# Kernel tuning notes

Measured on AMD Instinct MI355X. Metric: run time of the kernel, lower is better.

Reference implementation:

```python
import jax, jax.numpy as jnp
import numpy as np

N, E, F_DIM, H = 50000, 800000, 128, 4


def setup_inputs() -> dict:
    key = jax.random.key(0)
    ks = jax.random.split(key, 12)
    x = jax.random.normal(ks[0], (N, F_DIM), dtype=jnp.float32)
    edge_index = jax.random.randint(ks[1], (2, E), 0, N, dtype=jnp.int64)
    s = 1.0 / np.sqrt(F_DIM)
    return {
        "x": x,
        "edge_index": edge_index,
        "W_gat": jax.random.normal(ks[2], (F_DIM, H * F_DIM), dtype=jnp.float32) * s,
        "att_src": jax.random.normal(ks[3], (H, F_DIM), dtype=jnp.float32) * s,
        "att_dst": jax.random.normal(ks[4], (H, F_DIM), dtype=jnp.float32) * s,
        "bias_gat": jnp.zeros((H * F_DIM,), dtype=jnp.float32),
        "W_mha": jax.random.normal(ks[5], (H * F_DIM, F_DIM), dtype=jnp.float32) * s,
        "b_mha": jnp.zeros((F_DIM,), dtype=jnp.float32),
        "W1": jax.random.normal(ks[6], (F_DIM, F_DIM), dtype=jnp.float32) * s,
        "b1": jnp.zeros((F_DIM,), dtype=jnp.float32),
        "W2": jax.random.normal(ks[7], (F_DIM, F_DIM), dtype=jnp.float32) * s,
        "b2": jnp.zeros((F_DIM,), dtype=jnp.float32),
    }


def gat_conv(x, src, dst, W_gat, att_src, att_dst, bias_gat):
    n = x.shape[0]
    xp = (x @ W_gat).reshape(n, H, F_DIM)            # [N,H,F]
    a_src = jnp.einsum('nhf,hf->nh', xp, att_src)    # [N,H]
    a_dst = jnp.einsum('nhf,hf->nh', xp, att_dst)
    alpha = jax.nn.leaky_relu(a_src[src] + a_dst[dst], 0.2)  # [E,H]
    m = jax.ops.segment_max(alpha, dst, num_segments=n)      # segment softmax over dst
    e = jnp.exp(alpha - m[dst])
    denom = jax.ops.segment_sum(e, dst, num_segments=n)
    att = e / denom[dst]                              # [E,H]
    msg = xp[src] * att[:, :, None]                   # [E,H,F] gather-weight
    out = jax.ops.segment_sum(msg, dst, num_segments=n)  # [N,H,F]
    return out.reshape(n, H * F_DIM) + bias_gat


def reference(x, edge_index, W_gat, att_src, att_dst, bias_gat, W_mha, b_mha, W1, b1, W2, b2):
    n = x.shape[0]
    # PyG GATConv default add_self_loops=True
    ar = jnp.arange(n, dtype=edge_index.dtype)
    src = jnp.concatenate([edge_index[0], ar])
    dst = jnp.concatenate([edge_index[1], ar])
    residual = x
    h = jax.nn.leaky_relu(gat_conv(x, src, dst, W_gat, att_src, att_dst, bias_gat), 0.01)
    h = h @ W_mha + b_mha + residual
    # Ffn
    res2 = h
    h = jax.nn.leaky_relu(h @ W1 + b1, 0.01)
    h = h @ W2 + b2 + res2
    return h
```

## Files before the change

### kernel.cpp

```cpp
#include <hip/hip_runtime.h>

#define FD 128
#define NH 4
#define HF 512
#define CAP 64

typedef __attribute__((ext_vector_type(8))) short short8;
typedef __attribute__((ext_vector_type(4))) float v4f;

__device__ __forceinline__ float lrelu(float x, float s) { return x > 0.f ? x : s * x; }

__device__ __forceinline__ unsigned short f2bf(float f) {
    unsigned int u = __float_as_uint(f);
    u += 0x7FFFu + ((u >> 16) & 1u);
    return (unsigned short)(u >> 16);
}
__device__ __forceinline__ unsigned int pack2(float a, float b) {
    return (unsigned)f2bf(a) | ((unsigned)f2bf(b) << 16);
}

__global__ __launch_bounds__(256) void k_prep(const float* __restrict__ x,
                                              unsigned short* __restrict__ xb,
                                              const float* __restrict__ Wg, unsigned short* __restrict__ WgT,
                                              const float* __restrict__ Wm, unsigned short* __restrict__ WmT,
                                              const float* __restrict__ W1, unsigned short* __restrict__ W1T,
                                              const float* __restrict__ W2, unsigned short* __restrict__ W2T,
                                              const float* __restrict__ att_s,
                                              const float* __restrict__ att_d,
                                              float* __restrict__ U, int n) {
    const int t = threadIdx.x;
    int b = blockIdx.x;
    const int nCast = (n * FD / 8 + 255) / 256;
    const int nT1 = (FD * HF / 4 + 255) / 256;
    const int nT3 = (FD * FD / 4 + 255) / 256;
    if (b < nCast) {
        int i = b * 256 + t;
        if (i < n * FD / 8) {
            const float4* x4 = reinterpret_cast<const float4*>(x);
            float4 v0 = x4[i * 2], v1 = x4[i * 2 + 1];
            uint4 o;
            o.x = pack2(v0.x, v0.y); o.y = pack2(v0.z, v0.w);
            o.z = pack2(v1.x, v1.y); o.w = pack2(v1.z, v1.w);
            reinterpret_cast<uint4*>(xb)[i] = o;
        }
        return;
    }
    b -= nCast;
    if (b < nT1) {
        int i4 = (b * 256 + t) * 4;
        if (i4 < FD * HF) {
            int nn = i4 >> 7, k = i4 & 127;
            uint2 o;
            o.x = pack2(Wg[(size_t)k * HF + nn], Wg[(size_t)(k + 1) * HF + nn]);
            o.y = pack2(Wg[(size_t)(k + 2) * HF + nn], Wg[(size_t)(k + 3) * HF + nn]);
            *reinterpret_cast<uint2*>(&WgT[i4]) = o;
        }
        return;
    }
    b -= nT1;
    if (b < nT1) {
        int i4 = (b * 256 + t) * 4;
        if (i4 < HF * FD) {
            int nn = i4 >> 9, k = i4 & 511;
            uint2 o;
            o.x = pack2(Wm[(size_t)k * FD + nn], Wm[(size_t)(k + 1) * FD + nn]);
            o.y = pack2(Wm[(size_t)(k + 2) * FD + nn], Wm[(size_t)(k + 3) * FD + nn]);
            *reinterpret_cast<uint2*>(&WmT[i4]) = o;
        }
        return;
    }
    b -= nT1;
    if (b < nT3) {
        int i4 = (b * 256 + t) * 4;
        if (i4 < FD * FD) {
            int nn = i4 >> 7, k = i4 & 127;
            uint2 o;
            o.x = pack2(W1[(size_t)k * FD + nn], W1[(size_t)(k + 1) * FD + nn]);
            o.y = pack2(W1[(size_t)(k + 2) * FD + nn], W1[(size_t)(k + 3) * FD + nn]);
            *reinterpret_cast<uint2*>(&W1T[i4]) = o;
        }
        return;
    }
    b -= nT3;
    if (b < nT3) {
        int i4 = (b * 256 + t) * 4;
        if (i4 < FD * FD) {
            int nn = i4 >> 7, k = i4 & 127;
            uint2 o;
            o.x = pack2(W2[(size_t)k * FD + nn], W2[(size_t)(k + 1) * FD + nn]);
            o.y = pack2(W2[(size_t)(k + 2) * FD + nn], W2[(size_t)(k + 3) * FD + nn]);
            *reinterpret_cast<uint2*>(&W2T[i4]) = o;
        }
        return;
    }
    b -= nT3;
    {
        int idx = b * 256 + t;
        if (idx < 1024) {
            int type = idx >> 9, h = (idx >> 7) & 3, k = idx & 127;
            const float* att = type ? att_d : att_s;
            const float* wrow = &Wg[(size_t)k * HF + h * FD];
            const float* arow = &att[h * FD];
            float s = 0.f;
#pragma unroll 4
            for (int j = 0; j < FD; ++j) s += wrow[j] * arow[j];
            U[idx] = s;
        }
    }
}

__global__ __launch_bounds__(256) void k_alog(const unsigned short* __restrict__ xb,
                                              const float* __restrict__ U,
                                              float* __restrict__ a_s,
                                              float* __restrict__ a_d, int n) {
    int idx = blockIdx.x * 256 + threadIdx.x;
    int node = idx >> 2, h = idx & 3;
    if (node >= n) return;
    const uint4* xr = reinterpret_cast<const uint4*>(&xb[(size_t)node * FD]);
    const float* us = &U[h * FD];
    const float* ud = &U[512 + h * FD];
    float ps = 0.f, pd = 0.f;
#pragma unroll 4
    for (int j = 0; j < 16; ++j) {
        uint4 u = xr[j];
        const unsigned w[4] = {u.x, u.y, u.z, u.w};
#pragma unroll
        for (int q = 0; q < 4; ++q) {
            float f0 = __uint_as_float(w[q] << 16);
            float f1 = __uint_as_float(w[q] & 0xffff0000u);
            int c = j * 8 + q * 2;
            ps += f0 * us[c] + f1 * us[c + 1];
            pd += f0 * ud[c] + f1 * ud[c + 1];
        }
    }
    a_s[node * NH + h] = ps;
    a_d[node * NH + h] = pd;
}

__global__ __launch_bounds__(256) void k_scatter(const int* __restrict__ es,
                                                 const int* __restrict__ ed,
                                                 const float* __restrict__ a_s,
                                                 const float* __restrict__ a_d,
                                                 int* __restrict__ cur,
                                                 uint4* __restrict__ edata, int E, int n) {
    int i = blockIdx.x * 256 + threadIdx.x;
    if (i >= E) return;
    int s = es[i], d = ed[i];
    const float4 as = *reinterpret_cast<const float4*>(&a_s[(size_t)s * NH]);
    const float4 ad = *reinterpret_cast<const float4*>(&a_d[(size_t)d * NH]);
    float w0 = __expf(lrelu(as.x + ad.x, 0.2f));
    float w1 = __expf(lrelu(as.y + ad.y, 0.2f));
    float w2 = __expf(lrelu(as.z + ad.z, 0.2f));
    float w3 = __expf(lrelu(as.w + ad.w, 0.2f));
    int pos = atomicAdd(&cur[d], 1);
    if (pos < CAP) {
        uint4 r;
        r.x = (unsigned)s;
        r.y = pack2(w0, w1);
        r.z = pack2(w2, w3);
        r.w = 0u;
        edata[(size_t)d * CAP + pos] = r;
    }
}

#define GATH(REC) (*reinterpret_cast<const unsigned*>(&xb[(size_t)(int)(REC).x * FD + 2 * l]))
#define ACCUM(REC, U) do {                                                     \
    float w0_ = __uint_as_float((REC).y << 16);                                \
    float w1_ = __uint_as_float((REC).y & 0xffff0000u);                        \
    float w2_ = __uint_as_float((REC).z << 16);                                \
    float w3_ = __uint_as_float((REC).z & 0xffff0000u);                        \
    float g0_ = __uint_as_float((U) << 16);                                    \
    float g1_ = __uint_as_float((U) & 0xffff0000u);                            \
    ax0 += g0_ * w0_; ay0 += g1_ * w0_; den0 += w0_;                           \
    ax1 += g0_ * w1_; ay1 += g1_ * w1_; den1 += w1_;                           \
    ax2 += g0_ * w2_; ay2 += g1_ * w2_; den2 += w2_;                           \
    ax3 += g0_ * w3_; ay3 += g1_ * w3_; den3 += w3_;                           \
} while (0)

__global__ __launch_bounds__(256, 8) void k_aggr2(const unsigned short* __restrict__ xb,
                                                  const float* __restrict__ a_s,
                                                  const float* __restrict__ a_d,
                                                  const int* __restrict__ cur,
                                                  const uint4* __restrict__ edata,
                                                  unsigned short* __restrict__ agg, int n) {
    const int wv = threadIdx.x >> 6, l = threadIdx.x & 63;
    const int node = blockIdx.x * 4 + wv;
    if (node >= n) return;
    const int un = __builtin_amdgcn_readfirstlane(node);

    const float4 as4 = *reinterpret_cast<const float4*>(&a_s[(size_t)node * NH]);
    const float4 ad4 = *reinterpret_cast<const float4*>(&a_d[(size_t)node * NH]);
    const float wS0 = __expf(lrelu(as4.x + ad4.x, 0.2f));
    const float wS1 = __expf(lrelu(as4.y + ad4.y, 0.2f));
    const float wS2 = __expf(lrelu(as4.z + ad4.z, 0.2f));
    const float wS3 = __expf(lrelu(as4.w + ad4.w, 0.2f));

    float ax0, ay0, ax1, ay1, ax2, ay2, ax3, ay3;
    float den0 = wS0, den1 = wS1, den2 = wS2, den3 = wS3;
    {
        unsigned ux = *reinterpret_cast<const unsigned*>(&xb[(size_t)node * FD + 2 * l]);
        float f0 = __uint_as_float(ux << 16);
        float f1 = __uint_as_float(ux & 0xffff0000u);
        ax0 = f0 * wS0; ay0 = f1 * wS0;
        ax1 = f0 * wS1; ay1 = f1 * wS1;
        ax2 = f0 * wS2; ay2 = f1 * wS2;
        ax3 = f0 * wS3; ay3 = f1 * wS3;
    }

    const uint4* p = edata + (size_t)un * CAP;
    int dg = __builtin_amdgcn_readfirstlane(cur[un]);
    dg = min(dg, CAP);
    int e = 0;
    for (; e + 8 <= dg; e += 8) {
        uint4 r0 = p[e], r1 = p[e + 1], r2 = p[e + 2], r3 = p[e + 3];
        uint4 r4 = p[e + 4], r5 = p[e + 5], r6 = p[e + 6], r7 = p[e + 7];
        unsigned u0 = GATH(r0), u1 = GATH(r1), u2 = GATH(r2), u3 = GATH(r3);
        unsigned u4 = GATH(r4), u5 = GATH(r5), u6 = GATH(r6), u7 = GATH(r7);
        ACCUM(r0, u0); ACCUM(r1, u1); ACCUM(r2, u2); ACCUM(r3, u3);
        ACCUM(r4, u4); ACCUM(r5, u5); ACCUM(r6, u6); ACCUM(r7, u7);
    }
    if (e + 4 <= dg) {
        uint4 r0 = p[e], r1 = p[e + 1], r2 = p[e + 2], r3 = p[e + 3];
        unsigned u0 = GATH(r0), u1 = GATH(r1), u2 = GATH(r2), u3 = GATH(r3);
        ACCUM(r0, u0); ACCUM(r1, u1); ACCUM(r2, u2); ACCUM(r3, u3);
        e += 4;
    }
    if (e + 2 <= dg) {
        uint4 r0 = p[e], r1 = p[e + 1];
        unsigned u0 = GATH(r0), u1 = GATH(r1);
        ACCUM(r0, u0); ACCUM(r1, u1);
        e += 2;
    }
    if (e < dg) {
        uint4 r0 = p[e];
        unsigned u0 = GATH(r0);
        ACCUM(r0, u0);
    }

    const float i0 = 1.f / den0, i1 = 1.f / den1, i2 = 1.f / den2, i3 = 1.f / den3;
    unsigned* ag = reinterpret_cast<unsigned*>(&agg[(size_t)node * HF + 2 * l]);
    ag[0]   = pack2(ax0 * i0, ay0 * i0);
    ag[64]  = pack2(ax1 * i1, ay1 * i1);
    ag[128] = pack2(ax2 * i2, ay2 * i2);
    ag[192] = pack2(ax3 * i3, ay3 * i3);
}

#define PREFETCH8(BP, STRIDE) do {                                             \
    _Pragma("unroll")                                                          \
    for (int rnd = 0; rnd < 8; ++rnd) {                                        \
        int r_ = rnd * 16 + sr;                                                \
        R[rnd] = *reinterpret_cast<const short8*>(&(BP)[(size_t)r_ * (STRIDE) + sc]); \
    } } while (0)

#define COMMIT8() do {                                                         \
    __syncthreads();                                                           \
    _Pragma("unroll")                                                          \
    for (int rnd = 0; rnd < 8; ++rnd) {                                        \
        int r_ = rnd * 16 + sr;                                                \
        *reinterpret_cast<short8*>(&WL[r_][sc]) = R[rnd];                      \
    }                                                                          \
    __syncthreads(); } while (0)

#define LOAD_A(HH) do {                                                        \
    _Pragma("unroll")                                                          \
    for (int kk = 0; kk < 4; ++kk) {                                           \
        RA0[kk] = *reinterpret_cast<const short8*>(                            \
            &agg[(size_t)amr0 * HF + (HH) * FD + kk * 32 + kg]);               \
        RA1[kk] = *reinterpret_cast<const short8*>(                            \
            &agg[(size_t)amr1 * HF + (HH) * FD + kk * 32 + kg]);               \
    } } while (0)

__global__ __launch_bounds__(256, 2) void k_tail(const unsigned short* __restrict__ agg,
                                                 const unsigned short* __restrict__ WgT,
                                                 const float* __restrict__ biasg,
                                                 const unsigned short* __restrict__ WmT,
                                                 const float* __restrict__ bm,
                                                 const float* __restrict__ x,
                                                 const unsigned short* __restrict__ W1T,
                                                 const float* __restrict__ b1,
                                                 const unsigned short* __restrict__ W2T,
                                                 const float* __restrict__ b2,
                                                 float* __restrict__ out, int n) {
    __shared__ unsigned short WL[128][132];
    __shared__ unsigned short tS[128][132];
    const int tid = threadIdx.x;
    const int m0 = blockIdx.x * 128;
    const int wv = tid >> 6, l = tid & 63;
    const int rA = l & 15;
    const int kg = (l >> 4) * 8;
    const int mw = m0 + wv * 32;
    const int amr0 = min(mw + rA, n - 1);
    const int amr1 = min(mw + 16 + rA, n - 1);
    const int sr = tid >> 4, sc = (tid & 15) * 8;

    short8 R[8];
    short8 RA0[4], RA1[4];
    v4f hma[2][8];
#pragma unroll
    for (int g = 0; g < 2; ++g)
#pragma unroll
        for (int t = 0; t < 8; ++t) hma[g][t] = (v4f){0.f, 0.f, 0.f, 0.f};

    LOAD_A(0);
    PREFETCH8(WgT, FD);

#pragma unroll
    for (int h = 0; h < 4; ++h) {
        COMMIT8();
        PREFETCH8(WmT + h * FD, HF);
        v4f acc[2][8];
#pragma unroll
        for (int g = 0; g < 2; ++g)
#pragma unroll
            for (int t = 0; t < 8; ++t) acc[g][t] = (v4f){0.f, 0.f, 0.f, 0.f};
        __builtin_amdgcn_s_setprio(1);
#pragma unroll
        for (int kk = 0; kk < 4; ++kk) {
#pragma unroll
            for (int nt = 0; nt < 8; ++nt) {
                short8 b = *reinterpret_cast<const short8*>(&WL[nt * 16 + rA][kk * 32 + kg]);
                acc[0][nt] = __builtin_amdgcn_mfma_f32_16x16x32_bf16(RA0[kk], b, acc[0][nt], 0, 0, 0);
                acc[1][nt] = __builtin_amdgcn_mfma_f32_16x16x32_bf16(RA1[kk], b, acc[1][nt], 0, 0, 0);
            }
        }
        __builtin_amdgcn_s_setprio(0);
#pragma unroll
        for (int g = 0; g < 2; ++g)
#pragma unroll
            for (int nt = 0; nt < 8; ++nt) {
                const int col = nt * 16 + rA;
                const float bv = biasg[h * FD + col];
#pragma unroll
                for (int i = 0; i < 4; ++i)
                    tS[wv * 32 + g * 16 + (l >> 4) * 4 + i][col] =
                        f2bf(lrelu(acc[g][nt][i] + bv, 0.01f));
            }
        COMMIT8();
        PREFETCH8((h < 3 ? WgT + (h + 1) * FD * FD : W1T), FD);
        if (h < 3) LOAD_A(h + 1);
        __builtin_amdgcn_s_setprio(1);
#pragma unroll
        for (int kk = 0; kk < 4; ++kk) {
            short8 a0 = *reinterpret_cast<const short8*>(&tS[wv * 32 + rA][kk * 32 + kg]);
            short8 a1 = *reinterpret_cast<const short8*>(&tS[wv * 32 + 16 + rA][kk * 32 + kg]);
#pragma unroll
            for (int nt = 0; nt < 8; ++nt) {
                short8 b = *reinterpret_cast<const short8*>(&WL[nt * 16 + rA][kk * 32 + kg]);
                hma[0][nt] = __builtin_amdgcn_mfma_f32_16x16x32_bf16(a0, b, hma[0][nt], 0, 0, 0);
                hma[1][nt] = __builtin_amdgcn_mfma_f32_16x16x32_bf16(a1, b, hma[1][nt], 0, 0, 0);
            }
        }
        __builtin_amdgcn_s_setprio(0);
    }

#pragma unroll
    for (int g = 0; g < 2; ++g)
#pragma unroll
        for (int nt = 0; nt < 8; ++nt) {
            const int col = nt * 16 + rA;
            const float bv = bm[col];
#pragma unroll
            for (int i = 0; i < 4; ++i) {
                const int r = min(mw + g * 16 + (l >> 4) * 4 + i, n - 1);
                float v = hma[g][nt][i] + bv + x[(size_t)r * FD + col];
                hma[g][nt][i] = v;
                tS[wv * 32 + g * 16 + (l >> 4) * 4 + i][col] = f2bf(v);
            }
        }
    COMMIT8();
    PREFETCH8(W2T, FD);
    v4f acc[2][8];
#pragma unroll
    for (int g = 0; g < 2; ++g)
#pragma unroll
        for (int t = 0; t < 8; ++t) acc[g][t] = (v4f){0.f, 0.f, 0.f, 0.f};
    __builtin_amdgcn_s_setprio(1);
#pragma unroll
    for (int kk = 0; kk < 4; ++kk) {
        short8 a0 = *reinterpret_cast<const short8*>(&tS[wv * 32 + rA][kk * 32 + kg]);
        short8 a1 = *reinterpret_cast<const short8*>(&tS[wv * 32 + 16 + rA][kk * 32 + kg]);
#pragma unroll
        for (int nt = 0; nt < 8; ++nt) {
            short8 b = *reinterpret_cast<const short8*>(&WL[nt * 16 + rA][kk * 32 + kg]);
            acc[0][nt] = __builtin_amdgcn_mfma_f32_16x16x32_bf16(a0, b, acc[0][nt], 0, 0, 0);
            acc[1][nt] = __builtin_amdgcn_mfma_f32_16x16x32_bf16(a1, b, acc[1][nt], 0, 0, 0);
        }
    }
    __builtin_amdgcn_s_setprio(0);
#pragma unroll
    for (int g = 0; g < 2; ++g)
#pragma unroll
        for (int nt = 0; nt < 8; ++nt) {
            const int col = nt * 16 + rA;
            const float bv = b1[col];
#pragma unroll
            for (int i = 0; i < 4; ++i)
                tS[wv * 32 + g * 16 + (l >> 4) * 4 + i][col] =
                    f2bf(lrelu(acc[g][nt][i] + bv, 0.01f));
        }
    COMMIT8();
#pragma unroll
    for (int g = 0; g < 2; ++g)
#pragma unroll
        for (int t = 0; t < 8; ++t) acc[g][t] = (v4f){0.f, 0.f, 0.f, 0.f};
    __builtin_amdgcn_s_setprio(1);
#pragma unroll
    for (int kk = 0; kk < 4; ++kk) {
        short8 a0 = *reinterpret_cast<const short8*>(&tS[wv * 32 + rA][kk * 32 + kg]);
        short8 a1 = *reinterpret_cast<const short8*>(&tS[wv * 32 + 16 + rA][kk * 32 + kg]);
#pragma unroll
        for (int nt = 0; nt < 8; ++nt) {
            short8 b = *reinterpret_cast<const short8*>(&WL[nt * 16 + rA][kk * 32 + kg]);
            acc[0][nt] = __builtin_amdgcn_mfma_f32_16x16x32_bf16(a0, b, acc[0][nt], 0, 0, 0);
            acc[1][nt] = __builtin_amdgcn_mfma_f32_16x16x32_bf16(a1, b, acc[1][nt], 0, 0, 0);
        }
    }
    __builtin_amdgcn_s_setprio(0);
#pragma unroll
    for (int g = 0; g < 2; ++g)
#pragma unroll
        for (int nt = 0; nt < 8; ++nt) {
            const int col = nt * 16 + rA;
            const float bv = b2[col];
#pragma unroll
            for (int i = 0; i < 4; ++i) {
                const int r = mw + g * 16 + (l >> 4) * 4 + i;
                if (r < n)
                    out[(size_t)r * FD + col] = acc[g][nt][i] + bv + hma[g][nt][i];
            }
        }
}

extern "C" void kernel_launch(void* const* d_in, const int* in_sizes, int n_in,
                              void* d_out, int out_size, void* d_ws, size_t ws_size,
                              hipStream_t stream) {
    const float* x     = (const float*)d_in[0];
    const int*   ei    = (const int*)d_in[1];
    const float* Wg    = (const float*)d_in[2];
    const float* att_s = (const float*)d_in[3];
    const float* att_d = (const float*)d_in[4];
    const float* biasg = (const float*)d_in[5];
    const float* Wm    = (const float*)d_in[6];
    const float* bm    = (const float*)d_in[7];
    const float* W1    = (const float*)d_in[8];
    const float* b1    = (const float*)d_in[9];
    const float* W2    = (const float*)d_in[10];
    const float* b2    = (const float*)d_in[11];
    float* out = (float*)d_out;

    const int n = in_sizes[0] / FD;
    const int E = in_sizes[1] / 2;
    const int* esrc = ei;
    const int* edst = ei + E;

    char* w = (char*)d_ws;
    size_t o = 0;
    auto alloc = [&](size_t b) { void* p = w + o; o = (o + b + 255) & ~(size_t)255; return p; };
    unsigned short* x_b  = (unsigned short*)alloc((size_t)n * FD * 2);
    unsigned short* WgT  = (unsigned short*)alloc((size_t)FD * HF * 2);
    unsigned short* WmT  = (unsigned short*)alloc((size_t)HF * FD * 2);
    unsigned short* W1T  = (unsigned short*)alloc((size_t)FD * FD * 2);
    unsigned short* W2T  = (unsigned short*)alloc((size_t)FD * FD * 2);
    float*          U    = (float*)alloc(1024 * 4);
    unsigned short* aggb = (unsigned short*)alloc((size_t)n * HF * 2);
    float* a_s   = (float*)alloc((size_t)n * NH * 4);
    float* a_d   = (float*)alloc((size_t)n * NH * 4);
    int*   cur   = (int*)alloc((size_t)n * 4);
    uint4* edata = (uint4*)alloc((size_t)n * CAP * 16);

    hipMemsetAsync(cur, 0, (size_t)n * 4, stream);

    const int nCast = (n * FD / 8 + 255) / 256;
    const int nT1 = (FD * HF / 4 + 255) / 256;
    const int nT3 = (FD * FD / 4 + 255) / 256;
    k_prep<<<nCast + 2 * nT1 + 2 * nT3 + 4, 256, 0, stream>>>(
        x, x_b, Wg, WgT, Wm, WmT, W1, W1T, W2, W2T, att_s, att_d, U, n);

    k_alog<<<(n * 4 + 255) / 256, 256, 0, stream>>>(x_b, U, a_s, a_d, n);

    k_scatter<<<(E + 255) / 256, 256, 0, stream>>>(esrc, edst, a_s, a_d, cur, edata, E, n);
    k_aggr2<<<(n + 3) / 4, 256, 0, stream>>>(x_b, a_s, a_d, cur, edata, aggb, n);

    const int mb2 = (n + 127) / 128;
    k_tail<<<mb2, 256, 0, stream>>>(aggb, WgT, biasg, WmT, bm, x, W1T, b1, W2T, b2, out, n);
}
```

Before: 174.8 us.

## Partition scatter and aggregation by destination range across eight XCD slices

Blocks are mapped so that blockIdx modulo 8 picks one of eight contiguous destination-node ranges. In both the edge scatter and the aggregation kernel, each XCD should then touch only its own slice of the edge buckets and counters, which keeps that data in the local L2. The cost is that the scatter now launches eight times as many blocks, each reading every edge's destination index and discarding seven eighths of them. This relies on the round-robin assignment of blocks to XCDs.

```diff
diff --git a/kernel.cpp b/kernel.cpp
--- a/kernel.cpp
+++ b/kernel.cpp
@@ -142,10 +142,17 @@
                                                  const float* __restrict__ a_s,
                                                  const float* __restrict__ a_d,
                                                  int* __restrict__ cur,
-                                                 uint4* __restrict__ edata, int E, int n) {
-    int i = blockIdx.x * 256 + threadIdx.x;
+                                                 uint4* __restrict__ edata,
+                                                 int E, int n, int NPX) {
+    const int r = blockIdx.x & 7;
+    const int chunk = blockIdx.x >> 3;
+    const int lo = r * NPX;
+    const int hi = min(lo + NPX, n);
+    int i = chunk * 256 + threadIdx.x;
     if (i >= E) return;
-    int s = es[i], d = ed[i];
+    int d = ed[i];
+    if (d < lo || d >= hi) return;
+    int s = es[i];
     const float4 as = *reinterpret_cast<const float4*>(&a_s[(size_t)s * NH]);
     const float4 ad = *reinterpret_cast<const float4*>(&a_d[(size_t)d * NH]);
     float w0 = __expf(lrelu(as.x + ad.x, 0.2f));
@@ -154,12 +161,12 @@
     float w3 = __expf(lrelu(as.w + ad.w, 0.2f));
     int pos = atomicAdd(&cur[d], 1);
     if (pos < CAP) {
-        uint4 r;
-        r.x = (unsigned)s;
-        r.y = pack2(w0, w1);
-        r.z = pack2(w2, w3);
-        r.w = 0u;
-        edata[(size_t)d * CAP + pos] = r;
+        uint4 rr;
+        rr.x = (unsigned)s;
+        rr.y = pack2(w0, w1);
+        rr.z = pack2(w2, w3);
+        rr.w = 0u;
+        edata[(size_t)d * CAP + pos] = rr;
     }
 }
 
@@ -182,10 +189,13 @@
                                                   const float* __restrict__ a_d,
                                                   const int* __restrict__ cur,
                                                   const uint4* __restrict__ edata,
-                                                  unsigned short* __restrict__ agg, int n) {
+                                                  unsigned short* __restrict__ agg,
+                                                  int n, int NPX) {
     const int wv = threadIdx.x >> 6, l = threadIdx.x & 63;
-    const int node = blockIdx.x * 4 + wv;
-    if (node >= n) return;
+    const int r = blockIdx.x & 7, j = blockIdx.x >> 3;
+    const int node = r * NPX + j * 4 + wv;
+    const int hi = min(r * NPX + NPX, n);
+    if (node >= hi) return;
     const int un = __builtin_amdgcn_readfirstlane(node);
 
     const float4 as4 = *reinterpret_cast<const float4*>(&a_s[(size_t)node * NH]);
@@ -470,6 +480,7 @@
 
     hipMemsetAsync(cur, 0, (size_t)n * 4, stream);
 
+    const int NPX = (n + 7) / 8;
     const int nCast = (n * FD / 8 + 255) / 256;
     const int nT1 = (FD * HF / 4 + 255) / 256;
     const int nT3 = (FD * FD / 4 + 255) / 256;
@@ -478,8 +489,10 @@
 
     k_alog<<<(n * 4 + 255) / 256, 256, 0, stream>>>(x_b, U, a_s, a_d, n);
 
-    k_scatter<<<(E + 255) / 256, 256, 0, stream>>>(esrc, edst, a_s, a_d, cur, edata, E, n);
-    k_aggr2<<<(n + 3) / 4, 256, 0, stream>>>(x_b, a_s, a_d, cur, edata, aggb, n);
+    const int NB = (E + 255) / 256;
+    k_scatter<<<8 * NB, 256, 0, stream>>>(esrc, edst, a_s, a_d, cur, edata, E, n, NPX);
+    const int GPX = (NPX + 3) / 4;
+    k_aggr2<<<8 * GPX, 256, 0, stream>>>(x_b, a_s, a_d, cur, edata, aggb, n, NPX);
 
     const int mb2 = (n + 127) / 128;
     k_tail<<<mb2, 256, 0, stream>>>(aggb, WgT, biasg, WmT, bm, x, W1T, b1, W2T, b2, out, n);
```

Result: no change. 172.6 us (-1.2%).
